# Kernel optimization log

Hardware: AMD Instinct MI355X
Metric: run time of the kernel (lower is better)

Reference implementation:

```python
import jax, jax.numpy as jnp
import numpy as np

N = 50000          # total nodes
E = 800000         # edges (avg degree 16)
IN = 128           # in_feat
HID = 64           # hidden per head
HEADS = (4, 4, 1)
NEG_SLOPE = 0.2    # DGL GATConv leaky_relu default


def setup_inputs() -> dict:
    key = jax.random.key(0)
    ks = jax.random.split(key, 16)

    def w(k, shape, fan_in):
        return jax.random.normal(k, shape, jnp.float32) / np.float32(np.sqrt(fan_in))

    inp = {
        "feat": jax.random.normal(ks[0], (N, IN), jnp.float32),
        "src": jax.random.randint(ks[1], (E,), 0, N, jnp.int32),
        "dst": jax.random.randint(ks[2], (E,), 0, N, jnp.int32),
    }
    dims = [(IN, HEADS[0]), (HID * HEADS[0], HEADS[1]), (HID * HEADS[1], HEADS[2])]
    j = 3
    for i, (din, h) in enumerate(dims, 1):
        inp[f"W{i}"] = w(ks[j], (din, h * HID), din); j += 1
        inp[f"al{i}"] = w(ks[j], (h, HID), HID); j += 1
        inp[f"ar{i}"] = w(ks[j], (h, HID), HID); j += 1
        inp[f"b{i}"] = jnp.zeros((h * HID,), jnp.float32)
    return inp


def gat_layer(x, W, al, ar, b, src, dst, n_heads):
    # DGL GATConv: linear -> per-node attn logits -> edge leaky_relu ->
    # per-dst segment softmax -> weighted scatter-sum -> + bias
    h = (x @ W).reshape(N, n_heads, HID)                     # [N,H,D]
    el = jnp.einsum("nhd,hd->nh", h, al)                     # [N,H]
    er = jnp.einsum("nhd,hd->nh", h, ar)                     # [N,H]
    e = jax.nn.leaky_relu(el[src] + er[dst], NEG_SLOPE)      # [E,H]
    m = jax.ops.segment_max(e, dst, num_segments=N)          # [N,H]
    m = jnp.where(jnp.isfinite(m), m, 0.0)                   # empty segments -> -inf
    ex = jnp.exp(e - m[dst])                                 # [E,H]
    s = jax.ops.segment_sum(ex, dst, num_segments=N)         # [N,H]
    alpha = ex / s[dst]                                      # [E,H]
    msg = h[src] * alpha[:, :, None]                         # [E,H,D]
    out = jax.ops.segment_sum(msg, dst, num_segments=N)      # [N,H,D]
    return out + b.reshape(1, n_heads, HID)


def reference(feat, src, dst, W1, al1, ar1, b1, W2, al2, ar2, b2, W3, al3, ar3, b3):
    h = jax.nn.elu(gat_layer(feat, W1, al1, ar1, b1, src, dst, HEADS[0]))
    h = h.reshape(N, HEADS[0] * HID)                         # flatten heads
    h = jax.nn.elu(gat_layer(h, W2, al2, ar2, b2, src, dst, HEADS[1]))
    h = h.reshape(N, HEADS[1] * HID)
    h = gat_layer(h, W3, al3, ar3, b3, src, dst, HEADS[2])   # no activation
    return h.mean(axis=1)                                    # [N, HID]
```

## Files before the change

kernel.cpp:

```cpp
#include <hip/hip_runtime.h>
#include <math.h>

#define HID 64
#define NSLOPE 0.2f
#define SB 512
#define EXCAP 256

typedef __attribute__((ext_vector_type(8))) short short8v;
typedef __attribute__((ext_vector_type(4))) float float4v;

__device__ inline unsigned short f2bf(float x) {
  unsigned u = __float_as_uint(x);
  u += 0x7fffu + ((u >> 16) & 1u);
  return (unsigned short)(u >> 16);
}
__device__ inline float bf2f(unsigned short h) {
  return __uint_as_float(((unsigned)h) << 16);
}
__device__ inline float bflo(unsigned u) { return __uint_as_float(u << 16); }
__device__ inline float bfhi(unsigned u) { return __uint_as_float(u & 0xffff0000u); }

__global__ __launch_bounds__(256) void k_split(const float* __restrict__ x,
    unsigned short* __restrict__ hi, unsigned short* __restrict__ lo, int n) {
  int i = blockIdx.x * 256 + threadIdx.x;
  if (i < n) {
    float v = x[i];
    unsigned short h = f2bf(v);
    hi[i] = h;
    lo[i] = f2bf(v - bf2f(h));
  }
}

__global__ __launch_bounds__(256) void k_wsplit(const float* __restrict__ W,
    unsigned short* __restrict__ Whi, unsigned short* __restrict__ Wlo, int K, int N) {
  int i = blockIdx.x * 256 + threadIdx.x;
  if (i < N * K) {
    int n = i / K, k = i - n * K;
    float v = W[(size_t)k * N + n];
    unsigned short h = f2bf(v);
    Whi[i] = h;
    Wlo[i] = f2bf(v - bf2f(h));
  }
}

__global__ __launch_bounds__(256) void gemm_split(
    const unsigned short* __restrict__ Ahi, const unsigned short* __restrict__ Alo,
    const unsigned short* __restrict__ Bhi, const unsigned short* __restrict__ Blo,
    float* __restrict__ C, unsigned short* __restrict__ Gp, int M, int Nc, int K, int H) {
  __shared__ __align__(16) unsigned short AsHi[128 * 40];
  __shared__ __align__(16) unsigned short AsLo[128 * 40];
  __shared__ __align__(16) unsigned short BsHi[128 * 40];
  __shared__ __align__(16) unsigned short BsLo[128 * 40];
  const int tid = threadIdx.x;
  const int lane = tid & 63, wid = tid >> 6;
  const int wr = wid >> 1, wc = wid & 1;
  const int row0 = blockIdx.y * 128;
  const int col0 = blockIdx.x * 128;
  float4v acc[4][4];
  #pragma unroll
  for (int mi = 0; mi < 4; ++mi)
    #pragma unroll
    for (int ni = 0; ni < 4; ++ni)
      acc[mi][ni] = (float4v){0.f, 0.f, 0.f, 0.f};

  const int sr = tid >> 2;
  const int sc8 = (tid & 3) * 8;
  const int lr = lane & 15, lk = (lane >> 4) * 8;

  for (int k0 = 0; k0 < K; k0 += 32) {
    #pragma unroll
    for (int half = 0; half < 2; ++half) {
      int row = sr + half * 64;
      int arow = row0 + row; if (arow > M - 1) arow = M - 1;
      int brow = col0 + row; if (brow > Nc - 1) brow = Nc - 1;
      *(short8v*)&AsHi[row * 40 + sc8] = *(const short8v*)&Ahi[(size_t)arow * K + k0 + sc8];
      *(short8v*)&AsLo[row * 40 + sc8] = *(const short8v*)&Alo[(size_t)arow * K + k0 + sc8];
      *(short8v*)&BsHi[row * 40 + sc8] = *(const short8v*)&Bhi[(size_t)brow * K + k0 + sc8];
      *(short8v*)&BsLo[row * 40 + sc8] = *(const short8v*)&Blo[(size_t)brow * K + k0 + sc8];
    }
    __syncthreads();
    short8v ah[4], alv[4], bh[4], bl[4];
    #pragma unroll
    for (int mi = 0; mi < 4; ++mi) {
      int r = wr * 64 + mi * 16 + lr;
      ah[mi]  = *(const short8v*)&AsHi[r * 40 + lk];
      alv[mi] = *(const short8v*)&AsLo[r * 40 + lk];
    }
    #pragma unroll
    for (int ni = 0; ni < 4; ++ni) {
      int r = wc * 64 + ni * 16 + lr;
      bh[ni] = *(const short8v*)&BsHi[r * 40 + lk];
      bl[ni] = *(const short8v*)&BsLo[r * 40 + lk];
    }
    #pragma unroll
    for (int mi = 0; mi < 4; ++mi)
      #pragma unroll
      for (int ni = 0; ni < 4; ++ni) {
        acc[mi][ni] = __builtin_amdgcn_mfma_f32_16x16x32_bf16(ah[mi], bh[ni], acc[mi][ni], 0, 0, 0);
        acc[mi][ni] = __builtin_amdgcn_mfma_f32_16x16x32_bf16(ah[mi], bl[ni], acc[mi][ni], 0, 0, 0);
        acc[mi][ni] = __builtin_amdgcn_mfma_f32_16x16x32_bf16(alv[mi], bh[ni], acc[mi][ni], 0, 0, 0);
      }
    __syncthreads();
  }
  #pragma unroll
  for (int mi = 0; mi < 4; ++mi) {
    int rbase = row0 + wr * 64 + mi * 16 + (lane >> 4) * 4;
    #pragma unroll
    for (int ni = 0; ni < 4; ++ni) {
      int cc = col0 + wc * 64 + ni * 16 + (lane & 15);
      if (cc < Nc) {
        int gcol = (cc & 63) * H + (cc >> 6);
        #pragma unroll
        for (int q = 0; q < 4; ++q) {
          int rr = rbase + q;
          if (rr < M) {
            float v = acc[mi][ni][q];
            C[(size_t)rr * Nc + cc] = v;
            Gp[(size_t)rr * Nc + gcol] = f2bf(v);
          }
        }
      }
    }
  }
}

__global__ __launch_bounds__(256) void elr_kernel(const float* __restrict__ h,
    const float* __restrict__ al, const float* __restrict__ ar,
    float* __restrict__ el, float* __restrict__ er, int H, int N) {
  int n = blockIdx.x * 4 + (threadIdx.x >> 6);
  int lane = threadIdx.x & 63;
  if (n >= N) return;
  const float* hr = h + (size_t)n * H * HID;
  for (int hh = 0; hh < H; ++hh) {
    float v = hr[hh * HID + lane];
    float a = v * al[hh * HID + lane];
    float b = v * ar[hh * HID + lane];
    #pragma unroll
    for (int o = 32; o > 0; o >>= 1) { a += __shfl_xor(a, o); b += __shfl_xor(b, o); }
    if (lane == 0) { el[n * H + hh] = a; er[n * H + hh] = b; }
  }
}

__global__ void k_count(const int* __restrict__ dst, int* __restrict__ deg, int E) {
  int e = blockIdx.x * blockDim.x + threadIdx.x;
  if (e < E) atomicAdd(&deg[dst[e]], 1);
}
__global__ __launch_bounds__(SB) void k_blocksums(const int* __restrict__ deg,
                                                  int* __restrict__ bsums, int n) {
  __shared__ int s[SB];
  int t = threadIdx.x, i = blockIdx.x * SB + t;
  s[t] = (i < n) ? deg[i] : 0;
  __syncthreads();
  for (int o = SB >> 1; o > 0; o >>= 1) { if (t < o) s[t] += s[t + o]; __syncthreads(); }
  if (t == 0) bsums[blockIdx.x] = s[0];
}
__global__ __launch_bounds__(SB) void k_scancarry(const int* __restrict__ bsums,
                                                   int* __restrict__ carry, int nb) {
  __shared__ int s[SB];
  int t = threadIdx.x;
  int v = (t < nb) ? bsums[t] : 0;
  s[t] = v; __syncthreads();
  for (int o = 1; o < SB; o <<= 1) {
    int u = (t >= o) ? s[t - o] : 0;
    __syncthreads(); s[t] += u; __syncthreads();
  }
  if (t < nb) carry[t] = s[t] - v;
}
__global__ __launch_bounds__(SB) void k_offsets(const int* __restrict__ deg,
    const int* __restrict__ carry, int* __restrict__ offs, int n, int E) {
  __shared__ int s[SB];
  int t = threadIdx.x, i = blockIdx.x * SB + t;
  int v = (i < n) ? deg[i] : 0;
  s[t] = v; __syncthreads();
  for (int o = 1; o < SB; o <<= 1) {
    int u = (t >= o) ? s[t - o] : 0;
    __syncthreads(); s[t] += u; __syncthreads();
  }
  if (i < n) offs[i] = carry[blockIdx.x] + s[t] - v;
  if (i == n) offs[n] = E;
}
__global__ void k_fill(const int* __restrict__ src, const int* __restrict__ dst,
                       const int* __restrict__ offs, int* __restrict__ cursor,
                       int* __restrict__ esrc, int E) {
  int e = blockIdx.x * blockDim.x + threadIdx.x;
  if (e < E) {
    int d = dst[e];
    int slot = offs[d] + atomicAdd(&cursor[d], 1);
    esrc[slot] = src[e];
  }
}

template<int H, bool DO_ELU, bool SPLITOUT>
__global__ __launch_bounds__(256) void agg_kernel(const unsigned short* __restrict__ gp,
    const float* __restrict__ el, const float* __restrict__ er,
    const int* __restrict__ offs, const int* __restrict__ esrc,
    const float* __restrict__ bias,
    unsigned short* __restrict__ outHi, unsigned short* __restrict__ outLo,
    float* __restrict__ outF, int N) {
  __shared__ __align__(16) float exs_all[4][EXCAP * H];
  const int wv = threadIdx.x >> 6;
  const int n = blockIdx.x * 4 + wv;
  const int lane = threadIdx.x & 63;
  if (n >= N) return;
  float* exs = exs_all[wv];
  const int off = offs[n];
  const int deg = offs[n + 1] - off;
  float ern[H];
  if (H == 4) {
    float4 R = *(const float4*)&er[n * 4];
    ern[0] = R.x; ern[1] = R.y; ern[2] = R.z; ern[3] = R.w;
  } else {
    ern[0] = er[n];
  }
  float sum[H];
  #pragma unroll
  for (int h = 0; h < H; ++h) sum[h] = 0.f;
  for (int base = 0; base < deg; base += 64) {
    int i = base + lane;
    if (i < deg) {
      int s = esrc[off + i];
      if (H == 4) {
        float4 L = *(const float4*)&el[s * 4];
        float lv[4] = {L.x, L.y, L.z, L.w};
        float exv[4];
        #pragma unroll
        for (int h = 0; h < 4; ++h) {
          float e = lv[h] + ern[h];
          e = e > 0.f ? e : NSLOPE * e;
          exv[h] = __expf(fminf(e, 80.f));
          sum[h] += exv[h];
        }
        if (i < EXCAP)
          *(float4*)&exs[i * 4] = make_float4(exv[0], exv[1], exv[2], exv[3]);
      } else {
        float e = el[s] + ern[0];
        e = e > 0.f ? e : NSLOPE * e;
        float x = __expf(fminf(e, 80.f));
        sum[0] += x;
        if (i < EXCAP) exs[i] = x;
      }
    }
  }
  float inv[H];
  #pragma unroll
  for (int h = 0; h < H; ++h) {
    float v = sum[h];
    #pragma unroll
    for (int o = 32; o > 0; o >>= 1) v += __shfl_xor(v, o);
    inv[h] = v > 0.f ? 1.f / v : 0.f;
  }
  asm volatile("s_waitcnt lgkmcnt(0)" ::: "memory");
  float acc[H];
  #pragma unroll
  for (int h = 0; h < H; ++h) acc[h] = 0.f;
  const int degc = deg < EXCAP ? deg : EXCAP;
  int t = 0;
  for (; t + 8 <= degc; t += 8) {
    int4 sa = *(const int4*)&esrc[off + t];
    int4 sb = *(const int4*)&esrc[off + t + 4];
    int s[8] = {sa.x, sa.y, sa.z, sa.w, sb.x, sb.y, sb.z, sb.w};
    if (H == 4) {
      uint2 g[8];
      #pragma unroll
      for (int j = 0; j < 8; ++j)
        g[j] = *(const uint2*)&gp[(size_t)s[j] * 256 + lane * 4];
      #pragma unroll
      for (int j = 0; j < 8; ++j) {
        float4 x = *(const float4*)&exs[(t + j) * 4];
        acc[0] = fmaf(bflo(g[j].x), x.x, acc[0]);
        acc[1] = fmaf(bfhi(g[j].x), x.y, acc[1]);
        acc[2] = fmaf(bflo(g[j].y), x.z, acc[2]);
        acc[3] = fmaf(bfhi(g[j].y), x.w, acc[3]);
      }
    } else {
      unsigned short g[8];
      #pragma unroll
      for (int j = 0; j < 8; ++j) g[j] = gp[(size_t)s[j] * 64 + lane];
      #pragma unroll
      for (int j = 0; j < 8; ++j)
        acc[0] = fmaf(bf2f(g[j]), exs[t + j], acc[0]);
    }
  }
  for (; t < degc; ++t) {
    int s = esrc[off + t];
    if (H == 4) {
      float4 x = *(const float4*)&exs[t * 4];
      uint2 g = *(const uint2*)&gp[(size_t)s * 256 + lane * 4];
      acc[0] = fmaf(bflo(g.x), x.x, acc[0]);
      acc[1] = fmaf(bfhi(g.x), x.y, acc[1]);
      acc[2] = fmaf(bflo(g.y), x.z, acc[2]);
      acc[3] = fmaf(bfhi(g.y), x.w, acc[3]);
    } else {
      acc[0] = fmaf(bf2f(gp[(size_t)s * 64 + lane]), exs[t], acc[0]);
    }
  }
  for (; t < deg; ++t) {
    int s = esrc[off + t];
    #pragma unroll
    for (int hh = 0; hh < H; ++hh) {
      float e = el[s * H + hh] + ern[hh];
      e = e > 0.f ? e : NSLOPE * e;
      float x = __expf(fminf(e, 80.f));
      float v = (H == 4) ? bf2f(gp[(size_t)s * 256 + lane * 4 + hh])
                         : bf2f(gp[(size_t)s * 64 + lane]);
      acc[hh] = fmaf(v, x, acc[hh]);
    }
  }
  #pragma unroll
  for (int hh = 0; hh < H; ++hh) {
    float v = fmaf(acc[hh], inv[hh], bias[hh * HID + lane]);
    if (DO_ELU) v = v > 0.f ? v : expm1f(v);
    size_t oi = (size_t)n * (H * HID) + hh * HID + lane;
    if (SPLITOUT) {
      unsigned short hb = f2bf(v);
      outHi[oi] = hb;
      outLo[oi] = f2bf(v - bf2f(hb));
    } else {
      outF[oi] = v;
    }
  }
}

extern "C" void kernel_launch(void* const* d_in, const int* in_sizes, int n_in,
                              void* d_out, int out_size, void* d_ws, size_t ws_size,
                              hipStream_t stream) {
  const float* feat = (const float*)d_in[0];
  const int* src = (const int*)d_in[1];
  const int* dst = (const int*)d_in[2];
  const float* W1 = (const float*)d_in[3];
  const float* al1 = (const float*)d_in[4];
  const float* ar1 = (const float*)d_in[5];
  const float* b1 = (const float*)d_in[6];
  const float* W2 = (const float*)d_in[7];
  const float* al2 = (const float*)d_in[8];
  const float* ar2 = (const float*)d_in[9];
  const float* b2 = (const float*)d_in[10];
  const float* W3 = (const float*)d_in[11];
  const float* al3 = (const float*)d_in[12];
  const float* ar3 = (const float*)d_in[13];
  const float* b3 = (const float*)d_in[14];
  const int N = in_sizes[0] / 128;
  const int E = in_sizes[1];

  char* w = (char*)d_ws;
  auto alloc = [&](size_t bytes) {
    void* p = (void*)w;
    w += (bytes + 255) & ~(size_t)255;
    return p;
  };
  unsigned short* pHi = (unsigned short*)alloc((size_t)N * 256 * 2);
  unsigned short* pLo = (unsigned short*)alloc((size_t)N * 256 * 2);
  float* Cbuf = (float*)alloc((size_t)N * 256 * 4);
  unsigned short* Gp = (unsigned short*)alloc((size_t)N * 256 * 2);
  float* el = (float*)alloc((size_t)N * 4 * 4);
  float* er = (float*)alloc((size_t)N * 4 * 4);
  int* deg = (int*)alloc((size_t)N * 4);
  int* cursor = (int*)alloc((size_t)N * 4);
  int* offs = (int*)alloc((size_t)(N + 1) * 4);
  int nb = (N + SB - 1) / SB;
  int* bsums = (int*)alloc((size_t)nb * 4);
  int* carry = (int*)alloc((size_t)nb * 4);
  int* esrc = (int*)alloc((size_t)E * 4);
  unsigned short* W1h = (unsigned short*)alloc((size_t)256 * 128 * 2);
  unsigned short* W1l = (unsigned short*)alloc((size_t)256 * 128 * 2);
  unsigned short* W2h = (unsigned short*)alloc((size_t)256 * 256 * 2);
  unsigned short* W2l = (unsigned short*)alloc((size_t)256 * 256 * 2);
  unsigned short* W3h = (unsigned short*)alloc((size_t)64 * 256 * 2);
  unsigned short* W3l = (unsigned short*)alloc((size_t)64 * 256 * 2);

  hipMemsetAsync(deg, 0, (size_t)N * 4, stream);
  hipMemsetAsync(cursor, 0, (size_t)N * 4, stream);
  int eb = (E + 255) / 256;
  k_count<<<eb, 256, 0, stream>>>(dst, deg, E);
  k_blocksums<<<nb, SB, 0, stream>>>(deg, bsums, N);
  k_scancarry<<<1, SB, 0, stream>>>(bsums, carry, nb);
  k_offsets<<<nb, SB, 0, stream>>>(deg, carry, offs, N, E);
  k_fill<<<eb, 256, 0, stream>>>(src, dst, offs, cursor, esrc, E);

  k_wsplit<<<(256 * 128 + 255) / 256, 256, 0, stream>>>(W1, W1h, W1l, 128, 256);
  k_wsplit<<<(256 * 256 + 255) / 256, 256, 0, stream>>>(W2, W2h, W2l, 256, 256);
  k_wsplit<<<(64 * 256 + 255) / 256, 256, 0, stream>>>(W3, W3h, W3l, 256, 64);

  k_split<<<((N * 128) + 255) / 256, 256, 0, stream>>>(feat, pHi, pLo, N * 128);

  int rg = (N + 127) / 128;
  int ng4 = (N + 3) / 4;
  gemm_split<<<dim3(2, rg), 256, 0, stream>>>(pHi, pLo, W1h, W1l, Cbuf, Gp, N, 256, 128, 4);
  elr_kernel<<<ng4, 256, 0, stream>>>(Cbuf, al1, ar1, el, er, 4, N);
  agg_kernel<4, true, true><<<ng4, 256, 0, stream>>>(Gp, el, er, offs, esrc, b1, pHi, pLo, nullptr, N);
  gemm_split<<<dim3(2, rg), 256, 0, stream>>>(pHi, pLo, W2h, W2l, Cbuf, Gp, N, 256, 256, 4);
  elr_kernel<<<ng4, 256, 0, stream>>>(Cbuf, al2, ar2, el, er, 4, N);
  agg_kernel<4, true, true><<<ng4, 256, 0, stream>>>(Gp, el, er, offs, esrc, b2, pHi, pLo, nullptr, N);
  gemm_split<<<dim3(1, rg), 256, 0, stream>>>(pHi, pLo, W3h, W3l, Cbuf, Gp, N, 64, 256, 1);
  elr_kernel<<<ng4, 256, 0, stream>>>(Cbuf, al3, ar3, el, er, 1, N);
  agg_kernel<1, false, false><<<ng4, 256, 0, stream>>>(Gp, el, er, offs, esrc, b3, nullptr, nullptr, (float*)d_out, N);
}
```

Measured before the change: 490.2 us.

## Split each wavefront across multiple nodes with wider per-lane gathers in aggregation

```diff
diff --git a/kernel.cpp b/kernel.cpp
--- a/kernel.cpp
+++ b/kernel.cpp
@@ -191,18 +191,21 @@
 }
 
 template<int H, bool DO_ELU, bool SPLITOUT>
-__global__ __launch_bounds__(256) void agg_kernel(const unsigned short* __restrict__ gp,
+__global__ __launch_bounds__(64) void agg_kernel(const unsigned short* __restrict__ gp,
     const float* __restrict__ el, const float* __restrict__ er,
     const int* __restrict__ offs, const int* __restrict__ esrc,
     const float* __restrict__ bias,
     unsigned short* __restrict__ outHi, unsigned short* __restrict__ outLo,
     float* __restrict__ outF, int N) {
-  __shared__ __align__(16) float exs_all[4][EXCAP * H];
-  const int wv = threadIdx.x >> 6;
-  const int n = blockIdx.x * 4 + wv;
-  const int lane = threadIdx.x & 63;
+  constexpr int LPN = (H == 4) ? 32 : 16;
+  constexpr int NPW = 64 / LPN;
+  __shared__ __align__(16) float exs_all[NPW][EXCAP * H];
+  const int lane = threadIdx.x;
+  const int grp = lane / LPN;
+  const int sl = lane % LPN;
+  const int n = blockIdx.x * NPW + grp;
   if (n >= N) return;
-  float* exs = exs_all[wv];
+  float* exs = exs_all[grp];
   const int off = offs[n];
   const int deg = offs[n + 1] - off;
   float ern[H];
@@ -215,8 +218,8 @@
   float sum[H];
   #pragma unroll
   for (int h = 0; h < H; ++h) sum[h] = 0.f;
-  for (int base = 0; base < deg; base += 64) {
-    int i = base + lane;
+  for (int base = 0; base < deg; base += LPN) {
+    int i = base + sl;
     if (i < deg) {
       int s = esrc[off + i];
       if (H == 4) {
@@ -246,77 +249,141 @@
   for (int h = 0; h < H; ++h) {
     float v = sum[h];
     #pragma unroll
-    for (int o = 32; o > 0; o >>= 1) v += __shfl_xor(v, o);
+    for (int o = LPN / 2; o > 0; o >>= 1) v += __shfl_xor(v, o);
     inv[h] = v > 0.f ? 1.f / v : 0.f;
   }
   asm volatile("s_waitcnt lgkmcnt(0)" ::: "memory");
-  float acc[H];
-  #pragma unroll
-  for (int h = 0; h < H; ++h) acc[h] = 0.f;
   const int degc = deg < EXCAP ? deg : EXCAP;
   int t = 0;
-  for (; t + 8 <= degc; t += 8) {
-    int4 sa = *(const int4*)&esrc[off + t];
-    int4 sb = *(const int4*)&esrc[off + t + 4];
-    int s[8] = {sa.x, sa.y, sa.z, sa.w, sb.x, sb.y, sb.z, sb.w};
-    if (H == 4) {
-      uint2 g[8];
-      #pragma unroll
-      for (int j = 0; j < 8; ++j)
-        g[j] = *(const uint2*)&gp[(size_t)s[j] * 256 + lane * 4];
-      #pragma unroll
-      for (int j = 0; j < 8; ++j) {
+  if (H == 4) {
+    float acc[8];
+    #pragma unroll
+    for (int k = 0; k < 8; ++k) acc[k] = 0.f;
+    for (; t + 4 <= degc; t += 4) {
+      int4 sa = *(const int4*)&esrc[off + t];
+      int s[4] = {sa.x, sa.y, sa.z, sa.w};
+      uint4 g[4];
+      #pragma unroll
+      for (int j = 0; j < 4; ++j)
+        g[j] = *(const uint4*)&gp[(size_t)s[j] * 256 + sl * 8];
+      #pragma unroll
+      for (int j = 0; j < 4; ++j) {
         float4 x = *(const float4*)&exs[(t + j) * 4];
         acc[0] = fmaf(bflo(g[j].x), x.x, acc[0]);
         acc[1] = fmaf(bfhi(g[j].x), x.y, acc[1]);
         acc[2] = fmaf(bflo(g[j].y), x.z, acc[2]);
         acc[3] = fmaf(bfhi(g[j].y), x.w, acc[3]);
-      }
-    } else {
-      unsigned short g[8];
-      #pragma unroll
-      for (int j = 0; j < 8; ++j) g[j] = gp[(size_t)s[j] * 64 + lane];
-      #pragma unroll
-      for (int j = 0; j < 8; ++j)
-        acc[0] = fmaf(bf2f(g[j]), exs[t + j], acc[0]);
-    }
-  }
-  for (; t < degc; ++t) {
-    int s = esrc[off + t];
-    if (H == 4) {
+        acc[4] = fmaf(bflo(g[j].z), x.x, acc[4]);
+        acc[5] = fmaf(bfhi(g[j].z), x.y, acc[5]);
+        acc[6] = fmaf(bflo(g[j].w), x.z, acc[6]);
+        acc[7] = fmaf(bfhi(g[j].w), x.w, acc[7]);
+      }
+    }
+    for (; t < degc; ++t) {
+      int s = esrc[off + t];
+      uint4 g = *(const uint4*)&gp[(size_t)s * 256 + sl * 8];
       float4 x = *(const float4*)&exs[t * 4];
-      uint2 g = *(const uint2*)&gp[(size_t)s * 256 + lane * 4];
       acc[0] = fmaf(bflo(g.x), x.x, acc[0]);
       acc[1] = fmaf(bfhi(g.x), x.y, acc[1]);
       acc[2] = fmaf(bflo(g.y), x.z, acc[2]);
       acc[3] = fmaf(bfhi(g.y), x.w, acc[3]);
-    } else {
-      acc[0] = fmaf(bf2f(gp[(size_t)s * 64 + lane]), exs[t], acc[0]);
-    }
-  }
-  for (; t < deg; ++t) {
-    int s = esrc[off + t];
-    #pragma unroll
-    for (int hh = 0; hh < H; ++hh) {
-      float e = el[s * H + hh] + ern[hh];
+      acc[4] = fmaf(bflo(g.z), x.x, acc[4]);
+      acc[5] = fmaf(bfhi(g.z), x.y, acc[5]);
+      acc[6] = fmaf(bflo(g.w), x.z, acc[6]);
+      acc[7] = fmaf(bfhi(g.w), x.w, acc[7]);
+    }
+    for (; t < deg; ++t) {
+      int s = esrc[off + t];
+      float4 L = *(const float4*)&el[s * 4];
+      float lv[4] = {L.x, L.y, L.z, L.w};
+      float xv[4];
+      #pragma unroll
+      for (int h = 0; h < 4; ++h) {
+        float e = lv[h] + ern[h];
+        e = e > 0.f ? e : NSLOPE * e;
+        xv[h] = __expf(fminf(e, 80.f));
+      }
+      uint4 g = *(const uint4*)&gp[(size_t)s * 256 + sl * 8];
+      acc[0] = fmaf(bflo(g.x), xv[0], acc[0]);
+      acc[1] = fmaf(bfhi(g.x), xv[1], acc[1]);
+      acc[2] = fmaf(bflo(g.y), xv[2], acc[2]);
+      acc[3] = fmaf(bfhi(g.y), xv[3], acc[3]);
+      acc[4] = fmaf(bflo(g.z), xv[0], acc[4]);
+      acc[5] = fmaf(bfhi(g.z), xv[1], acc[5]);
+      acc[6] = fmaf(bflo(g.w), xv[2], acc[6]);
+      acc[7] = fmaf(bfhi(g.w), xv[3], acc[7]);
+    }
+    #pragma unroll
+    for (int dd = 0; dd < 2; ++dd) {
+      int d = 2 * sl + dd;
+      #pragma unroll
+      for (int hh = 0; hh < 4; ++hh) {
+        float v = fmaf(acc[dd * 4 + hh], inv[hh], bias[hh * HID + d]);
+        if (DO_ELU) v = v > 0.f ? v : expm1f(v);
+        size_t oi = (size_t)n * 256 + hh * HID + d;
+        if (SPLITOUT) {
+          unsigned short hb = f2bf(v);
+          outHi[oi] = hb;
+          outLo[oi] = f2bf(v - bf2f(hb));
+        } else {
+          outF[oi] = v;
+        }
+      }
+    }
+  } else {
+    float acc[4];
+    #pragma unroll
+    for (int k = 0; k < 4; ++k) acc[k] = 0.f;
+    for (; t + 8 <= degc; t += 8) {
+      int4 sa = *(const int4*)&esrc[off + t];
+      int4 sb = *(const int4*)&esrc[off + t + 4];
+      int s[8] = {sa.x, sa.y, sa.z, sa.w, sb.x, sb.y, sb.z, sb.w};
+      uint2 g[8];
+      #pragma unroll
+      for (int j = 0; j < 8; ++j)
+        g[j] = *(const uint2*)&gp[(size_t)s[j] * 64 + sl * 4];
+      #pragma unroll
+      for (int j = 0; j < 8; ++j) {
+        float x = exs[t + j];
+        acc[0] = fmaf(bflo(g[j].x), x, acc[0]);
+        acc[1] = fmaf(bfhi(g[j].x), x, acc[1]);
+        acc[2] = fmaf(bflo(g[j].y), x, acc[2]);
+        acc[3] = fmaf(bfhi(g[j].y), x, acc[3]);
+      }
+    }
+    for (; t < degc; ++t) {
+      int s = esrc[off + t];
+      uint2 g = *(const uint2*)&gp[(size_t)s * 64 + sl * 4];
+      float x = exs[t];
+      acc[0] = fmaf(bflo(g.x), x, acc[0]);
+      acc[1] = fmaf(bfhi(g.x), x, acc[1]);
+      acc[2] = fmaf(bflo(g.y), x, acc[2]);
+      acc[3] = fmaf(bfhi(g.y), x, acc[3]);
+    }
+    for (; t < deg; ++t) {
+      int s = esrc[off + t];
+      float e = el[s] + ern[0];
       e = e > 0.f ? e : NSLOPE * e;
       float x = __expf(fminf(e, 80.f));
-      float v = (H == 4) ? bf2f(gp[(size_t)s * 256 + lane * 4 + hh])
-                         : bf2f(gp[(size_t)s * 64 + lane]);
-      acc[hh] = fmaf(v, x, acc[hh]);
-    }
-  }
-  #pragma unroll
-  for (int hh = 0; hh < H; ++hh) {
-    float v = fmaf(acc[hh], inv[hh], bias[hh * HID + lane]);
-    if (DO_ELU) v = v > 0.f ? v : expm1f(v);
-    size_t oi = (size_t)n * (H * HID) + hh * HID + lane;
-    if (SPLITOUT) {
-      unsigned short hb = f2bf(v);
-      outHi[oi] = hb;
-      outLo[oi] = f2bf(v - bf2f(hb));
-    } else {
-      outF[oi] = v;
+      uint2 g = *(const uint2*)&gp[(size_t)s * 64 + sl * 4];
+      acc[0] = fmaf(bflo(g.x), x, acc[0]);
+      acc[1] = fmaf(bfhi(g.x), x, acc[1]);
+      acc[2] = fmaf(bflo(g.y), x, acc[2]);
+      acc[3] = fmaf(bfhi(g.y), x, acc[3]);
+    }
+    #pragma unroll
+    for (int k = 0; k < 4; ++k) {
+      int d = 4 * sl + k;
+      float v = fmaf(acc[k], inv[0], bias[d]);
+      if (DO_ELU) v = v > 0.f ? v : expm1f(v);
+      size_t oi = (size_t)n * HID + d;
+      if (SPLITOUT) {
+        unsigned short hb = f2bf(v);
+        outHi[oi] = hb;
+        outLo[oi] = f2bf(v - bf2f(hb));
+      } else {
+        outF[oi] = v;
+      }
     }
   }
 }
@@ -385,13 +452,15 @@
 
   int rg = (N + 127) / 128;
   int ng4 = (N + 3) / 4;
+  int ag4 = (N + 1) / 2;
+  int ag1 = (N + 3) / 4;
   gemm_split<<<dim3(2, rg), 256, 0, stream>>>(pHi, pLo, W1h, W1l, Cbuf, Gp, N, 256, 128, 4);
   elr_kernel<<<ng4, 256, 0, stream>>>(Cbuf, al1, ar1, el, er, 4, N);
-  agg_kernel<4, true, true><<<ng4, 256, 0, stream>>>(Gp, el, er, offs, esrc, b1, pHi, pLo, nullptr, N);
+  agg_kernel<4, true, true><<<ag4, 64, 0, stream>>>(Gp, el, er, offs, esrc, b1, pHi, pLo, nullptr, N);
   gemm_split<<<dim3(2, rg), 256, 0, stream>>>(pHi, pLo, W2h, W2l, Cbuf, Gp, N, 256, 256, 4);
   elr_kernel<<<ng4, 256, 0, stream>>>(Cbuf, al2, ar2, el, er, 4, N);
-  agg_kernel<4, true, true><<<ng4, 256, 0, stream>>>(Gp, el, er, offs, esrc, b2, pHi, pLo, nullptr, N);
+  agg_kernel<4, true, true><<<ag4, 64, 0, stream>>>(Gp, el, er, offs, esrc, b2, pHi, pLo, nullptr, N);
   gemm_split<<<dim3(1, rg), 256, 0, stream>>>(pHi, pLo, W3h, W3l, Cbuf, Gp, N, 64, 256, 1);
   elr_kernel<<<ng4, 256, 0, stream>>>(Cbuf, al3, ar3, el, er, 1, N);
-  agg_kernel<1, false, false><<<ng4, 256, 0, stream>>>(Gp, el, er, offs, esrc, b3, nullptr, nullptr, (float*)d_out, N);
-}
+  agg_kernel<1, false, false><<<ag1, 64, 0, stream>>>(Gp, el, er, offs, esrc, b3, nullptr, nullptr, (float*)d_out, N);
+}
```

New measurement: 456.7 us. 6.8% less time.
